# Kernel tuning notes

Measured on AMD Instinct MI355X. Metric: run time of the kernel, lower is better.

## Reference

```python
import jax, jax.numpy as jnp
import numpy as np

N_NODES = 50000
N_FEAT = 128
N_EDGES = 1600000
HID = 64


def gcn_conv(x, row, col, w, W, b, n):
    """PyG GCNConv with edge weights and added self-loops (fill_value=1).
    x: [N, Fin]; row/col: [E] (src, dst); w: [E]; W: [Fin, Fout]; b: [Fout].
    """
    loop = jnp.arange(n)
    r = jnp.concatenate([row, loop])
    c = jnp.concatenate([col, loop])
    ww = jnp.concatenate([w, jnp.ones((n,), dtype=x.dtype)])
    deg = jax.ops.segment_sum(ww, c, num_segments=n)  # [N]
    dinv = jnp.where(deg > 0, jax.lax.rsqrt(deg), 0.0)
    norm = dinv[r] * ww * dinv[c]  # [E+N]
    xw = x @ W  # [N, Fout] -- linear before propagate, as in PyG
    msg = norm[:, None] * xw[r]  # gather + scale
    out = jax.ops.segment_sum(msg, c, num_segments=n)  # scatter-add
    return out + b


def setup_inputs() -> dict:
    key = jax.random.key(0)
    ks = jax.random.split(key, 12)
    features = jax.random.normal(ks[0], (N_NODES, N_FEAT), dtype=jnp.float32)
    edge_index = jax.random.randint(ks[1], (2, N_EDGES), 0, N_NODES, dtype=jnp.int64)
    edge_attr = jax.random.uniform(ks[2], (N_EDGES,), dtype=jnp.float32)
    s = 0.05
    # generator encoder: GCNConv(n_feat->64), GCNConv(64->n_feat)
    Wg1 = jax.random.normal(ks[3], (N_FEAT, HID), dtype=jnp.float32) * s
    bg1 = jnp.zeros((HID,), dtype=jnp.float32)
    Wg2 = jax.random.normal(ks[4], (HID, N_FEAT), dtype=jnp.float32) * s
    bg2 = jnp.zeros((N_FEAT,), dtype=jnp.float32)
    # discriminator: GCNConv(n_feat->64), Linear(n_nodes*64 -> 1)
    Wd1 = jax.random.normal(ks[5], (N_FEAT, HID), dtype=jnp.float32) * s
    bd1 = jnp.zeros((HID,), dtype=jnp.float32)
    wfc = jax.random.normal(ks[6], (N_NODES * HID,), dtype=jnp.float32) * 0.001
    bfc = jnp.zeros((), dtype=jnp.float32)
    return {"features": features, "edge_index": edge_index, "edge_attr": edge_attr,
            "Wg1": Wg1, "bg1": bg1, "Wg2": Wg2, "bg2": bg2,
            "Wd1": Wd1, "bd1": bd1, "wfc": wfc, "bfc": bfc}


def reference(features, edge_index, edge_attr, Wg1, bg1, Wg2, bg2, Wd1, bd1, wfc, bfc):
    n = features.shape[0]
    row, col = edge_index[0], edge_index[1]
    # --- generator encoder (eval mode: dropout is a no-op) ---
    h = gcn_conv(features, row, col, edge_attr, Wg1, bg1, n)
    h = jax.nn.relu(h)
    z = jax.nn.sigmoid(gcn_conv(h, row, col, edge_attr, Wg2, bg2, n))  # [N, n_feat]
    # --- GAE inner-product decoder over the given edge list ---
    edge_probs = jax.nn.sigmoid(jnp.sum(z[row] * z[col], axis=-1))  # [E]
    # residual connection
    enc = z + features
    edge_probs = jnp.nan_to_num(edge_probs, nan=0.0)
    # --- discriminator (eval mode: no noise, no dropout) ---
    d = gcn_conv(enc, row, col, edge_probs, Wd1, bd1, n)
    d = jax.nn.relu(d)
    logit = jnp.dot(d.reshape(-1), wfc) + bfc
    return jax.nn.sigmoid(logit)
```

## Files before the change

### kernel.cpp

```cpp
#include <hip/hip_runtime.h>
#include <math.h>

static constexpr int NN = 50000;
static constexpr int NF = 128;
static constexpr int NH = 64;
static constexpr int NE = 1600000;
static constexpr int NBUSED = (NN + 255) / 256;
static constexpr int NWG = 256;
static constexpr int CHUNK = NE / NWG;

typedef unsigned long long u64;
typedef float f32x2 __attribute__((ext_vector_type(2)));


__device__ __forceinline__ float bf2f(unsigned u) { return __uint_as_float(u << 16); }
__device__ __forceinline__ unsigned short f2bf(float f) {
  unsigned b = __float_as_uint(f);
  b += 0x7fffu + ((b >> 16) & 1u);
  return (unsigned short)(b >> 16);
}
__device__ __forceinline__ float sigm(float x) { return 1.f / (1.f + __expf(-x)); }
__device__ __forceinline__ unsigned char f2fp8(float f) {
  int v = __builtin_amdgcn_cvt_pk_fp8_f32(f, f, 0, false);
  return (unsigned char)(v & 0xff);
}
__device__ __forceinline__ void fp8x16_dec(uint4 v, float* o) {
  f32x2 t;
  t = __builtin_amdgcn_cvt_pk_f32_fp8(v.x, false); o[0] = t.x;  o[1] = t.y;
  t = __builtin_amdgcn_cvt_pk_f32_fp8(v.x, true);  o[2] = t.x;  o[3] = t.y;
  t = __builtin_amdgcn_cvt_pk_f32_fp8(v.y, false); o[4] = t.x;  o[5] = t.y;
  t = __builtin_amdgcn_cvt_pk_f32_fp8(v.y, true);  o[6] = t.x;  o[7] = t.y;
  t = __builtin_amdgcn_cvt_pk_f32_fp8(v.z, false); o[8] = t.x;  o[9] = t.y;
  t = __builtin_amdgcn_cvt_pk_f32_fp8(v.z, true);  o[10] = t.x; o[11] = t.y;
  t = __builtin_amdgcn_cvt_pk_f32_fp8(v.w, false); o[12] = t.x; o[13] = t.y;
  t = __builtin_amdgcn_cvt_pk_f32_fp8(v.w, true);  o[14] = t.x; o[15] = t.y;
}
__device__ __forceinline__ uint4 fp8x16_enc(const float* o) {
  uint4 r;
  int v;
  v = __builtin_amdgcn_cvt_pk_fp8_f32(o[0], o[1], 0, false);
  v = __builtin_amdgcn_cvt_pk_fp8_f32(o[2], o[3], v, true);
  r.x = (unsigned)v;
  v = __builtin_amdgcn_cvt_pk_fp8_f32(o[4], o[5], 0, false);
  v = __builtin_amdgcn_cvt_pk_fp8_f32(o[6], o[7], v, true);
  r.y = (unsigned)v;
  v = __builtin_amdgcn_cvt_pk_fp8_f32(o[8], o[9], 0, false);
  v = __builtin_amdgcn_cvt_pk_fp8_f32(o[10], o[11], v, true);
  r.z = (unsigned)v;
  v = __builtin_amdgcn_cvt_pk_fp8_f32(o[12], o[13], 0, false);
  v = __builtin_amdgcn_cvt_pk_fp8_f32(o[14], o[15], v, true);
  r.w = (unsigned)v;
  return r;
}


__global__ __launch_bounds__(256) void bhist_k(const int* __restrict__ col,
                                               int* __restrict__ counts) {
  __shared__ int cnt[256];
  cnt[threadIdx.x] = 0;
  __syncthreads();
  int g = blockIdx.x;
  int e1 = g * CHUNK + CHUNK;
  for (int e = g * CHUNK + threadIdx.x; e < e1; e += 256)
    atomicAdd(&cnt[col[e] >> 8], 1);
  __syncthreads();
  counts[g * 256 + threadIdx.x] = cnt[threadIdx.x];
}

__global__ __launch_bounds__(256) void bscan_k(int* __restrict__ counts) {
  __shared__ int sm[256];
  int b = threadIdx.x;
  int tot = 0;
  for (int g = 0; g < NWG; g++) tot += counts[g * 256 + b];
  sm[b] = tot;
  __syncthreads();
  int v = tot;
  for (int off = 1; off < 256; off <<= 1) {
    int u = (b >= off) ? sm[b - off] : 0;
    __syncthreads();
    sm[b] += u;
    __syncthreads();
  }
  int run = sm[b] - v;
  for (int g = 0; g < NWG; g++) {
    int c = counts[g * 256 + b];
    counts[g * 256 + b] = run;
    run += c;
  }
}

__global__ __launch_bounds__(256) void bpart_k(const int* __restrict__ row,
                                               const int* __restrict__ col,
                                               const float* __restrict__ w,
                                               const int* __restrict__ counts,
                                               u64* __restrict__ ebuf) {
  __shared__ int cur[256];
  int g = blockIdx.x;
  cur[threadIdx.x] = counts[g * 256 + threadIdx.x];
  __syncthreads();
  int e1 = g * CHUNK + CHUNK;
  for (int e = g * CHUNK + threadIdx.x; e < e1; e += 256) {
    int c = col[e];
    int p = atomicAdd(&cur[c >> 8], 1);
    u64 pk = ((u64)(unsigned)__float_as_int(w[e]) << 32) |
             ((unsigned)(c & 255) << 16) | (unsigned)row[e];
    ebuf[p] = pk;
  }
}

__global__ __launch_bounds__(256) void bsortA_k(const u64* __restrict__ ebuf,
                                                const int* __restrict__ counts,
                                                int* __restrict__ rowstart,
                                                float* __restrict__ dinv) {
  __shared__ int cnt[256];
  __shared__ float deg[256];
  __shared__ int sm[256];
  int b = blockIdx.x, t = threadIdx.x;
  cnt[t] = 0;
  deg[t] = 1.0f;
  __syncthreads();
  int boff = counts[b];
  int bend = (b < NBUSED - 1) ? counts[b + 1] : NE;
  for (int e = boff + t; e < bend; e += 256) {
    u64 pk = ebuf[e];
    unsigned lo = (unsigned)pk;
    int c = (lo >> 16) & 255;
    atomicAdd(&cnt[c], 1);
    atomicAdd(&deg[c], __uint_as_float((unsigned)(pk >> 32)));
  }
  __syncthreads();
  int v = cnt[t];
  sm[t] = v;
  __syncthreads();
  for (int off = 1; off < 256; off <<= 1) {
    int u = (t >= off) ? sm[t - off] : 0;
    __syncthreads();
    sm[t] += u;
    __syncthreads();
  }
  int colg = b * 256 + t;
  if (colg < NN) {
    rowstart[colg] = boff + sm[t] - v;
    dinv[colg] = rsqrtf(deg[t]);
  }
  if (b == NBUSED - 1 && t == 0) rowstart[NN] = NE;
}

__global__ __launch_bounds__(256) void bsortB_k(const u64* __restrict__ ebuf,
                                                const int* __restrict__ counts,
                                                const int* __restrict__ rowstart,
                                                const float* __restrict__ dinv,
                                                int2* __restrict__ es) {
  __shared__ int cur[256];
  int b = blockIdx.x, t = threadIdx.x;
  int colg = b * 256 + t;
  cur[t] = (colg < NN) ? rowstart[colg] : NE;
  __syncthreads();
  int boff = counts[b];
  int bend = (b < NBUSED - 1) ? counts[b + 1] : NE;
  for (int e = boff + t; e < bend; e += 256) {
    u64 pk = ebuf[e];
    unsigned lo = (unsigned)pk;
    int r = lo & 0xffff;
    int c = (lo >> 16) & 255;
    float wv = __uint_as_float((unsigned)(pk >> 32));
    int p = atomicAdd(&cur[c], 1);
    es[p] = make_int2(r, __float_as_int(dinv[r] * wv));
  }
}

template<int K, int M, int ACT, bool OUTF, bool OUTH, bool XH, bool OUT8>
__global__ __launch_bounds__(256) void gemm_k(const float* __restrict__ X,
                                              const unsigned short* __restrict__ Xh,
                                              const float* __restrict__ Xadd,
                                              const float* __restrict__ W,
                                              const float* __restrict__ bias,
                                              float* __restrict__ Yf,
                                              unsigned short* __restrict__ Yh,
                                              unsigned char* __restrict__ Y8) {
  __shared__ float Ws[K * M];
  __shared__ float Xs[16][K];
  for (int i = threadIdx.x; i < K * M; i += 256) Ws[i] = W[i];
  int r0 = blockIdx.x * 16;
  for (int i = threadIdx.x; i < 16 * K; i += 256) {
    int r = i / K, k = i % K;
    size_t off = (size_t)(r0 + r) * K + k;
    float v = XH ? bf2f(Xh[off]) : X[off];
    if (Xadd) v += Xadd[off];
    Xs[r][k] = v;
  }
  __syncthreads();
  constexpr int RPT = 16 * M / 256;
  constexpr int RS = 256 / M;
  int colc = threadIdx.x % M;
  int rb = threadIdx.x / M;
  float acc[RPT];
#pragma unroll
  for (int i = 0; i < RPT; i++) acc[i] = 0.f;
  for (int k = 0; k < K; k++) {
    float wv = Ws[k * M + colc];
#pragma unroll
    for (int i = 0; i < RPT; i++) acc[i] += Xs[rb + i * RS][k] * wv;
  }
#pragma unroll
  for (int i = 0; i < RPT; i++) {
    int r = r0 + rb + i * RS;
    float o = acc[i];
    if (ACT > 0) o += bias[colc];
    if (ACT == 2) o = sigm(o);
    if (OUTF) Yf[(size_t)r * M + colc] = o;
    if (OUTH) Yh[(size_t)r * M + colc] = f2bf(o);
    if (OUT8) Y8[(size_t)r * M + colc] = f2fp8(o);
  }
}

template<int MODE>
__global__ __launch_bounds__(256) void agg64_k(const int* __restrict__ rowstart,
                                               const int2* __restrict__ es,
                                               const unsigned char* __restrict__ src8,
                                               const float* __restrict__ dinv,
                                               const float* __restrict__ bias,
                                               unsigned char* __restrict__ out8,
                                               float* __restrict__ outf,
                                               const float* __restrict__ wfc) {
  int wid = (blockIdx.x * 256 + threadIdx.x) >> 6;
  int lane = threadIdx.x & 63;
  int sub = lane >> 2;
  int l = lane & 3;
  int e0 = rowstart[wid], e1 = rowstart[wid + 1];
  float di = dinv[wid];
  float a[16];
#pragma unroll
  for (int c = 0; c < 16; c++) a[c] = 0.f;
  for (int eb = e0; eb < e1; eb += 16) {
    int e = eb + sub;
    bool valid = e < e1;
    int2 er = es[valid ? e : eb];
    float nm;
    if (MODE == 2) nm = valid ? dinv[er.x] * __int_as_float(er.y) : 0.f;
    else nm = valid ? __int_as_float(er.y) : 0.f;
    uint4 v = *(const uint4*)(src8 + (size_t)er.x * 64 + l * 16);
    float t[16];
    fp8x16_dec(v, t);
#pragma unroll
    for (int c = 0; c < 16; c++) a[c] = fmaf(nm, t[c], a[c]);
  }
#pragma unroll
  for (int c = 0; c < 16; c++) {
    a[c] += __shfl_xor(a[c], 4);
    a[c] += __shfl_xor(a[c], 8);
    a[c] += __shfl_xor(a[c], 16);
    a[c] += __shfl_xor(a[c], 32);
  }
  uint4 sv = *(const uint4*)(src8 + (size_t)wid * 64 + l * 16);
  float sf[16];
  fp8x16_dec(sv, sf);

  if (MODE == 0) {
    if (sub == 0) {
      float o[16];
#pragma unroll
      for (int c4 = 0; c4 < 4; c4++) {
        float4 b4 = *(const float4*)(bias + l * 16 + c4 * 4);
        o[c4 * 4 + 0] = fmaxf(di * (a[c4 * 4 + 0] + di * sf[c4 * 4 + 0]) + b4.x, 0.f);
        o[c4 * 4 + 1] = fmaxf(di * (a[c4 * 4 + 1] + di * sf[c4 * 4 + 1]) + b4.y, 0.f);
        o[c4 * 4 + 2] = fmaxf(di * (a[c4 * 4 + 2] + di * sf[c4 * 4 + 2]) + b4.z, 0.f);
        o[c4 * 4 + 3] = fmaxf(di * (a[c4 * 4 + 3] + di * sf[c4 * 4 + 3]) + b4.w, 0.f);
      }
      *(uint4*)(out8 + (size_t)wid * 64 + l * 16) = fp8x16_enc(o);
    }
  } else if (MODE == 1) {
    if (sub == 0) {
#pragma unroll
      for (int c4 = 0; c4 < 4; c4++) {
        float4 o4;
        o4.x = di * (a[c4 * 4 + 0] + di * sf[c4 * 4 + 0]);
        o4.y = di * (a[c4 * 4 + 1] + di * sf[c4 * 4 + 1]);
        o4.z = di * (a[c4 * 4 + 2] + di * sf[c4 * 4 + 2]);
        o4.w = di * (a[c4 * 4 + 3] + di * sf[c4 * 4 + 3]);
        *(float4*)(outf + (size_t)wid * 64 + l * 16 + c4 * 4) = o4;
      }
    }
  } else {
    float s = 0.f;
    if (sub == 0) {
#pragma unroll
      for (int c4 = 0; c4 < 4; c4++) {
        float4 b4 = *(const float4*)(bias + l * 16 + c4 * 4);
        float4 w4 = *(const float4*)(wfc + (size_t)wid * 64 + l * 16 + c4 * 4);
        float o0 = fmaxf(di * (a[c4 * 4 + 0] + di * sf[c4 * 4 + 0]) + b4.x, 0.f);
        float o1 = fmaxf(di * (a[c4 * 4 + 1] + di * sf[c4 * 4 + 1]) + b4.y, 0.f);
        float o2 = fmaxf(di * (a[c4 * 4 + 2] + di * sf[c4 * 4 + 2]) + b4.z, 0.f);
        float o3 = fmaxf(di * (a[c4 * 4 + 3] + di * sf[c4 * 4 + 3]) + b4.w, 0.f);
        s += o0 * w4.x + o1 * w4.y + o2 * w4.z + o3 * w4.w;
      }
    }
    s += __shfl_xor(s, 1);
    s += __shfl_xor(s, 2);
    __shared__ float bs[4];
    if (lane == 0) bs[threadIdx.x >> 6] = s;
    __syncthreads();
    if (threadIdx.x == 0) outf[blockIdx.x] = bs[0] + bs[1] + bs[2] + bs[3];
  }
}

__global__ __launch_bounds__(256) void eprob8_k(const int* __restrict__ rowstart,
                                                int2* __restrict__ es,
                                                const unsigned char* __restrict__ z8,
                                                float* __restrict__ dinv2) {
  int wid = (blockIdx.x * 256 + threadIdx.x) >> 6;
  int lane = threadIdx.x & 63;
  int sub = lane >> 3;
  int l = lane & 7;
  uint4 zv = *(const uint4*)(z8 + (size_t)wid * NF + l * 16);
  float zi[16];
  fp8x16_dec(zv, zi);
  int e0 = rowstart[wid], e1 = rowstart[wid + 1];
  float sum = 0.f;
  for (int eb = e0; eb < e1; eb += 8) {
    int e = eb + sub;
    bool valid = e < e1;
    int r = es[valid ? e : eb].x;
    uint4 v = *(const uint4*)(z8 + (size_t)r * NF + l * 16);
    float zr[16];
    fp8x16_dec(v, zr);
    float d = 0.f;
#pragma unroll
    for (int c = 0; c < 16; c++) d = fmaf(zr[c], zi[c], d);
    d += __shfl_xor(d, 1);
    d += __shfl_xor(d, 2);
    d += __shfl_xor(d, 4);
    if (valid && l == 0) {
      float p = sigm(d);
      es[e].y = __float_as_int(p);
      sum += p;
    }
  }
  sum += __shfl_xor(sum, 8);
  sum += __shfl_xor(sum, 16);
  sum += __shfl_xor(sum, 32);
  if (lane == 0) dinv2[wid] = rsqrtf(1.f + sum);
}

__global__ __launch_bounds__(256) void reduce_k(const float* __restrict__ partials, int n,
                                                const float* __restrict__ bfc,
                                                float* __restrict__ out) {
  float s = 0.f;
  for (int i = threadIdx.x; i < n; i += 256) s += partials[i];
  s += __shfl_xor(s, 1);
  s += __shfl_xor(s, 2);
  s += __shfl_xor(s, 4);
  s += __shfl_xor(s, 8);
  s += __shfl_xor(s, 16);
  s += __shfl_xor(s, 32);
  __shared__ float ws4[4];
  if ((threadIdx.x & 63) == 0) ws4[threadIdx.x >> 6] = s;
  __syncthreads();
  if (threadIdx.x == 0) out[0] = sigm(ws4[0] + ws4[1] + ws4[2] + ws4[3] + bfc[0]);
}


extern "C" void kernel_launch(void* const* d_in, const int* in_sizes, int n_in,
                              void* d_out, int out_size, void* d_ws, size_t ws_size,
                              hipStream_t stream) {
  const float* features = (const float*)d_in[0];
  const int* edge_index = (const int*)d_in[1];
  const float* edge_attr = (const float*)d_in[2];
  const float* Wg1 = (const float*)d_in[3];
  const float* bg1 = (const float*)d_in[4];
  const float* Wg2 = (const float*)d_in[5];
  const float* bg2 = (const float*)d_in[6];
  const float* Wd1 = (const float*)d_in[7];
  const float* bd1 = (const float*)d_in[8];
  const float* wfc = (const float*)d_in[9];
  const float* bfc = (const float*)d_in[10];
  float* out = (float*)d_out;

  const int* row = edge_index;
  const int* col = edge_index + NE;

  char* wsb = (char*)d_ws;
  auto carve = [&](size_t bytes) {
    void* p = wsb;
    wsb += (bytes + 255) & ~(size_t)255;
    return p;
  };
  int*   counts   = (int*)carve((size_t)NWG * 256 * 4);
  int*   rowstart = (int*)carve((NN + 1) * 4);
  float* dinv     = (float*)carve(NN * 4);
  float* dinv2    = (float*)carve(NN * 4);
  u64*   ebuf     = (u64*)carve((size_t)NE * 8);
  int2*  es       = (int2*)carve((size_t)NE * 8);
  unsigned char* xw8a = (unsigned char*)carve((size_t)NN * NH);
  unsigned char* hh8  = (unsigned char*)carve((size_t)NN * NH);
  float* ah   = (float*)carve((size_t)NN * NH * 4);
  unsigned short* zh = (unsigned short*)carve((size_t)NN * NF * 2);
  unsigned char* z8  = (unsigned char*)carve((size_t)NN * NF);
  unsigned char* xw8d = (unsigned char*)carve((size_t)NN * NH);
  float* partials = (float*)carve(12500 * 4);

  const int GG = NN / 16;
  const int GW = NN * 64 / 256;

  bhist_k<<<NWG, 256, 0, stream>>>(col, counts);
  bscan_k<<<1, 256, 0, stream>>>(counts);
  bpart_k<<<NWG, 256, 0, stream>>>(row, col, edge_attr, counts, ebuf);
  bsortA_k<<<NBUSED, 256, 0, stream>>>(ebuf, counts, rowstart, dinv);
  bsortB_k<<<NBUSED, 256, 0, stream>>>(ebuf, counts, rowstart, dinv, es);

  gemm_k<NF, NH, 0, false, false, false, true><<<GG, 256, 0, stream>>>(
      features, nullptr, nullptr, Wg1, nullptr, nullptr, nullptr, xw8a);
  agg64_k<0><<<GW, 256, 0, stream>>>(rowstart, es, xw8a, dinv, bg1, hh8, nullptr, nullptr);

  agg64_k<1><<<GW, 256, 0, stream>>>(rowstart, es, hh8, dinv, nullptr, nullptr, ah, nullptr);
  gemm_k<NH, NF, 2, false, true, false, true><<<GG, 256, 0, stream>>>(
      ah, nullptr, nullptr, Wg2, bg2, nullptr, zh, z8);

  eprob8_k<<<GW, 256, 0, stream>>>(rowstart, es, z8, dinv2);

  gemm_k<NF, NH, 0, false, false, true, true><<<GG, 256, 0, stream>>>(
      nullptr, zh, features, Wd1, nullptr, nullptr, nullptr, xw8d);
  agg64_k<2><<<GW, 256, 0, stream>>>(rowstart, es, xw8d, dinv2, bd1, nullptr, partials, wfc);

  reduce_k<<<1, 256, 0, stream>>>(partials, GW, bfc, out);
}
```

Before: 345.2 us.

## Pack edge records into 32 bits and assign six nodes per wave

Each sorted edge record now packs a 16-bit source index and a bf16 norm/probability into one 32-bit word instead of an int2, halving edge-stream traffic in the aggregation and edge-probability kernels. The aggregation and edge-probability kernels now have each wave loop over six consecutive destination nodes, reusing the row-start boundary and cutting launched waves and per-wave setup, with a launch-bounds occupancy hint. The trade-off is lost precision on edge weights and probabilities (bf16), and less parallelism plus more load imbalance per wave.

```diff
diff --git a/kernel.cpp b/kernel.cpp
--- a/kernel.cpp
+++ b/kernel.cpp
@@ -8,6 +8,9 @@
 static constexpr int NBUSED = (NN + 255) / 256;
 static constexpr int NWG = 256;
 static constexpr int CHUNK = NE / NWG;
+static constexpr int NPW = 6;
+static constexpr int NWAVES = (NN + NPW - 1) / NPW;
+static constexpr int GWC = (NWAVES * 64 + 255) / 256;
 
 typedef unsigned long long u64;
 typedef float f32x2 __attribute__((ext_vector_type(2)));
@@ -150,7 +153,7 @@
                                                 const int* __restrict__ counts,
                                                 const int* __restrict__ rowstart,
                                                 const float* __restrict__ dinv,
-                                                int2* __restrict__ es) {
+                                                unsigned* __restrict__ es4) {
   __shared__ int cur[256];
   int b = blockIdx.x, t = threadIdx.x;
   int colg = b * 256 + t;
@@ -165,7 +168,7 @@
     int c = (lo >> 16) & 255;
     float wv = __uint_as_float((unsigned)(pk >> 32));
     int p = atomicAdd(&cur[c], 1);
-    es[p] = make_int2(r, __float_as_int(dinv[r] * wv));
+    es4[p] = ((unsigned)f2bf(dinv[r] * wv) << 16) | (unsigned)r;
   }
 }
 
@@ -215,86 +218,96 @@
 }
 
 template<int MODE>
-__global__ __launch_bounds__(256) void agg64_k(const int* __restrict__ rowstart,
-                                               const int2* __restrict__ es,
-                                               const unsigned char* __restrict__ src8,
-                                               const float* __restrict__ dinv,
-                                               const float* __restrict__ bias,
-                                               unsigned char* __restrict__ out8,
-                                               float* __restrict__ outf,
-                                               const float* __restrict__ wfc) {
-  int wid = (blockIdx.x * 256 + threadIdx.x) >> 6;
+__global__ __launch_bounds__(256, 8) void agg64_k(const int* __restrict__ rowstart,
+                                                  const unsigned* __restrict__ es4,
+                                                  const unsigned char* __restrict__ src8,
+                                                  const float* __restrict__ dinv,
+                                                  const float* __restrict__ bias,
+                                                  unsigned char* __restrict__ out8,
+                                                  float* __restrict__ outf,
+                                                  const float* __restrict__ wfc) {
+  int w = (blockIdx.x * 256 + threadIdx.x) >> 6;
+  int n0 = w * NPW;
   int lane = threadIdx.x & 63;
   int sub = lane >> 2;
   int l = lane & 3;
-  int e0 = rowstart[wid], e1 = rowstart[wid + 1];
-  float di = dinv[wid];
-  float a[16];
-#pragma unroll
-  for (int c = 0; c < 16; c++) a[c] = 0.f;
-  for (int eb = e0; eb < e1; eb += 16) {
-    int e = eb + sub;
-    bool valid = e < e1;
-    int2 er = es[valid ? e : eb];
-    float nm;
-    if (MODE == 2) nm = valid ? dinv[er.x] * __int_as_float(er.y) : 0.f;
-    else nm = valid ? __int_as_float(er.y) : 0.f;
-    uint4 v = *(const uint4*)(src8 + (size_t)er.x * 64 + l * 16);
-    float t[16];
-    fp8x16_dec(v, t);
-#pragma unroll
-    for (int c = 0; c < 16; c++) a[c] = fmaf(nm, t[c], a[c]);
-  }
-#pragma unroll
-  for (int c = 0; c < 16; c++) {
-    a[c] += __shfl_xor(a[c], 4);
-    a[c] += __shfl_xor(a[c], 8);
-    a[c] += __shfl_xor(a[c], 16);
-    a[c] += __shfl_xor(a[c], 32);
-  }
-  uint4 sv = *(const uint4*)(src8 + (size_t)wid * 64 + l * 16);
-  float sf[16];
-  fp8x16_dec(sv, sf);
-
-  if (MODE == 0) {
-    if (sub == 0) {
-      float o[16];
-#pragma unroll
-      for (int c4 = 0; c4 < 4; c4++) {
-        float4 b4 = *(const float4*)(bias + l * 16 + c4 * 4);
-        o[c4 * 4 + 0] = fmaxf(di * (a[c4 * 4 + 0] + di * sf[c4 * 4 + 0]) + b4.x, 0.f);
-        o[c4 * 4 + 1] = fmaxf(di * (a[c4 * 4 + 1] + di * sf[c4 * 4 + 1]) + b4.y, 0.f);
-        o[c4 * 4 + 2] = fmaxf(di * (a[c4 * 4 + 2] + di * sf[c4 * 4 + 2]) + b4.z, 0.f);
-        o[c4 * 4 + 3] = fmaxf(di * (a[c4 * 4 + 3] + di * sf[c4 * 4 + 3]) + b4.w, 0.f);
+  float s = 0.f;
+  if (n0 < NN) {
+    int n1 = min(n0 + NPW, NN);
+    int e0 = rowstart[n0];
+    for (int wid = n0; wid < n1; ++wid) {
+      int e1 = rowstart[wid + 1];
+      float di = dinv[wid];
+      float a[16];
+#pragma unroll
+      for (int c = 0; c < 16; c++) a[c] = 0.f;
+      for (int eb = e0; eb < e1; eb += 16) {
+        int e = eb + sub;
+        bool valid = e < e1;
+        unsigned er = es4[valid ? e : eb];
+        int r = (int)(er & 0xffffu);
+        float nm;
+        if (MODE == 2) nm = valid ? dinv[r] * bf2f(er >> 16) : 0.f;
+        else nm = valid ? bf2f(er >> 16) : 0.f;
+        uint4 v = *(const uint4*)(src8 + (size_t)r * 64 + l * 16);
+        float t[16];
+        fp8x16_dec(v, t);
+#pragma unroll
+        for (int c = 0; c < 16; c++) a[c] = fmaf(nm, t[c], a[c]);
       }
-      *(uint4*)(out8 + (size_t)wid * 64 + l * 16) = fp8x16_enc(o);
+#pragma unroll
+      for (int c = 0; c < 16; c++) {
+        a[c] += __shfl_xor(a[c], 4);
+        a[c] += __shfl_xor(a[c], 8);
+        a[c] += __shfl_xor(a[c], 16);
+        a[c] += __shfl_xor(a[c], 32);
+      }
+      uint4 sv = *(const uint4*)(src8 + (size_t)wid * 64 + l * 16);
+      float sf[16];
+      fp8x16_dec(sv, sf);
+      if (MODE == 0) {
+        if (sub == 0) {
+          float o[16];
+#pragma unroll
+          for (int c4 = 0; c4 < 4; c4++) {
+            float4 b4 = *(const float4*)(bias + l * 16 + c4 * 4);
+            o[c4 * 4 + 0] = fmaxf(di * (a[c4 * 4 + 0] + di * sf[c4 * 4 + 0]) + b4.x, 0.f);
+            o[c4 * 4 + 1] = fmaxf(di * (a[c4 * 4 + 1] + di * sf[c4 * 4 + 1]) + b4.y, 0.f);
+            o[c4 * 4 + 2] = fmaxf(di * (a[c4 * 4 + 2] + di * sf[c4 * 4 + 2]) + b4.z, 0.f);
+            o[c4 * 4 + 3] = fmaxf(di * (a[c4 * 4 + 3] + di * sf[c4 * 4 + 3]) + b4.w, 0.f);
+          }
+          *(uint4*)(out8 + (size_t)wid * 64 + l * 16) = fp8x16_enc(o);
+        }
+      } else if (MODE == 1) {
+        if (sub == 0) {
+#pragma unroll
+          for (int c4 = 0; c4 < 4; c4++) {
+            float4 o4;
+            o4.x = di * (a[c4 * 4 + 0] + di * sf[c4 * 4 + 0]);
+            o4.y = di * (a[c4 * 4 + 1] + di * sf[c4 * 4 + 1]);
+            o4.z = di * (a[c4 * 4 + 2] + di * sf[c4 * 4 + 2]);
+            o4.w = di * (a[c4 * 4 + 3] + di * sf[c4 * 4 + 3]);
+            *(float4*)(outf + (size_t)wid * 64 + l * 16 + c4 * 4) = o4;
+          }
+        }
+      } else {
+        if (sub == 0) {
+#pragma unroll
+          for (int c4 = 0; c4 < 4; c4++) {
+            float4 b4 = *(const float4*)(bias + l * 16 + c4 * 4);
+            float4 w4 = *(const float4*)(wfc + (size_t)wid * 64 + l * 16 + c4 * 4);
+            float o0 = fmaxf(di * (a[c4 * 4 + 0] + di * sf[c4 * 4 + 0]) + b4.x, 0.f);
+            float o1 = fmaxf(di * (a[c4 * 4 + 1] + di * sf[c4 * 4 + 1]) + b4.y, 0.f);
+            float o2 = fmaxf(di * (a[c4 * 4 + 2] + di * sf[c4 * 4 + 2]) + b4.z, 0.f);
+            float o3 = fmaxf(di * (a[c4 * 4 + 3] + di * sf[c4 * 4 + 3]) + b4.w, 0.f);
+            s += o0 * w4.x + o1 * w4.y + o2 * w4.z + o3 * w4.w;
+          }
+        }
+      }
+      e0 = e1;
     }
-  } else if (MODE == 1) {
-    if (sub == 0) {
-#pragma unroll
-      for (int c4 = 0; c4 < 4; c4++) {
-        float4 o4;
-        o4.x = di * (a[c4 * 4 + 0] + di * sf[c4 * 4 + 0]);
-        o4.y = di * (a[c4 * 4 + 1] + di * sf[c4 * 4 + 1]);
-        o4.z = di * (a[c4 * 4 + 2] + di * sf[c4 * 4 + 2]);
-        o4.w = di * (a[c4 * 4 + 3] + di * sf[c4 * 4 + 3]);
-        *(float4*)(outf + (size_t)wid * 64 + l * 16 + c4 * 4) = o4;
-      }
-    }
-  } else {
-    float s = 0.f;
-    if (sub == 0) {
-#pragma unroll
-      for (int c4 = 0; c4 < 4; c4++) {
-        float4 b4 = *(const float4*)(bias + l * 16 + c4 * 4);
-        float4 w4 = *(const float4*)(wfc + (size_t)wid * 64 + l * 16 + c4 * 4);
-        float o0 = fmaxf(di * (a[c4 * 4 + 0] + di * sf[c4 * 4 + 0]) + b4.x, 0.f);
-        float o1 = fmaxf(di * (a[c4 * 4 + 1] + di * sf[c4 * 4 + 1]) + b4.y, 0.f);
-        float o2 = fmaxf(di * (a[c4 * 4 + 2] + di * sf[c4 * 4 + 2]) + b4.z, 0.f);
-        float o3 = fmaxf(di * (a[c4 * 4 + 3] + di * sf[c4 * 4 + 3]) + b4.w, 0.f);
-        s += o0 * w4.x + o1 * w4.y + o2 * w4.z + o3 * w4.w;
-      }
-    }
+  }
+  if (MODE == 2) {
     s += __shfl_xor(s, 1);
     s += __shfl_xor(s, 2);
     __shared__ float bs[4];
@@ -304,42 +317,50 @@
   }
 }
 
-__global__ __launch_bounds__(256) void eprob8_k(const int* __restrict__ rowstart,
-                                                int2* __restrict__ es,
-                                                const unsigned char* __restrict__ z8,
-                                                float* __restrict__ dinv2) {
-  int wid = (blockIdx.x * 256 + threadIdx.x) >> 6;
+__global__ __launch_bounds__(256, 8) void eprob8_k(const int* __restrict__ rowstart,
+                                                   unsigned* __restrict__ es4,
+                                                   const unsigned char* __restrict__ z8,
+                                                   float* __restrict__ dinv2) {
+  int w = (blockIdx.x * 256 + threadIdx.x) >> 6;
+  int n0 = w * NPW;
+  if (n0 >= NN) return;
+  int n1 = min(n0 + NPW, NN);
   int lane = threadIdx.x & 63;
   int sub = lane >> 3;
   int l = lane & 7;
-  uint4 zv = *(const uint4*)(z8 + (size_t)wid * NF + l * 16);
-  float zi[16];
-  fp8x16_dec(zv, zi);
-  int e0 = rowstart[wid], e1 = rowstart[wid + 1];
-  float sum = 0.f;
-  for (int eb = e0; eb < e1; eb += 8) {
-    int e = eb + sub;
-    bool valid = e < e1;
-    int r = es[valid ? e : eb].x;
-    uint4 v = *(const uint4*)(z8 + (size_t)r * NF + l * 16);
-    float zr[16];
-    fp8x16_dec(v, zr);
-    float d = 0.f;
-#pragma unroll
-    for (int c = 0; c < 16; c++) d = fmaf(zr[c], zi[c], d);
-    d += __shfl_xor(d, 1);
-    d += __shfl_xor(d, 2);
-    d += __shfl_xor(d, 4);
-    if (valid && l == 0) {
-      float p = sigm(d);
-      es[e].y = __float_as_int(p);
-      sum += p;
+  int e0 = rowstart[n0];
+  for (int wid = n0; wid < n1; ++wid) {
+    int e1 = rowstart[wid + 1];
+    uint4 zv = *(const uint4*)(z8 + (size_t)wid * NF + l * 16);
+    float zi[16];
+    fp8x16_dec(zv, zi);
+    float sum = 0.f;
+    for (int eb = e0; eb < e1; eb += 8) {
+      int e = eb + sub;
+      bool valid = e < e1;
+      unsigned er = es4[valid ? e : eb];
+      int r = (int)(er & 0xffffu);
+      uint4 v = *(const uint4*)(z8 + (size_t)r * NF + l * 16);
+      float zr[16];
+      fp8x16_dec(v, zr);
+      float d = 0.f;
+#pragma unroll
+      for (int c = 0; c < 16; c++) d = fmaf(zr[c], zi[c], d);
+      d += __shfl_xor(d, 1);
+      d += __shfl_xor(d, 2);
+      d += __shfl_xor(d, 4);
+      if (valid && l == 0) {
+        float p = sigm(d);
+        es4[e] = ((unsigned)f2bf(p) << 16) | (unsigned)r;
+        sum += p;
+      }
     }
-  }
-  sum += __shfl_xor(sum, 8);
-  sum += __shfl_xor(sum, 16);
-  sum += __shfl_xor(sum, 32);
-  if (lane == 0) dinv2[wid] = rsqrtf(1.f + sum);
+    sum += __shfl_xor(sum, 8);
+    sum += __shfl_xor(sum, 16);
+    sum += __shfl_xor(sum, 32);
+    if (lane == 0) dinv2[wid] = rsqrtf(1.f + sum);
+    e0 = e1;
+  }
 }
 
 __global__ __launch_bounds__(256) void reduce_k(const float* __restrict__ partials, int n,
@@ -390,37 +411,36 @@
   float* dinv     = (float*)carve(NN * 4);
   float* dinv2    = (float*)carve(NN * 4);
   u64*   ebuf     = (u64*)carve((size_t)NE * 8);
-  int2*  es       = (int2*)carve((size_t)NE * 8);
+  unsigned* es4   = (unsigned*)carve((size_t)NE * 4);
   unsigned char* xw8a = (unsigned char*)carve((size_t)NN * NH);
   unsigned char* hh8  = (unsigned char*)carve((size_t)NN * NH);
   float* ah   = (float*)carve((size_t)NN * NH * 4);
   unsigned short* zh = (unsigned short*)carve((size_t)NN * NF * 2);
   unsigned char* z8  = (unsigned char*)carve((size_t)NN * NF);
   unsigned char* xw8d = (unsigned char*)carve((size_t)NN * NH);
-  float* partials = (float*)carve(12500 * 4);
+  float* partials = (float*)carve((size_t)GWC * 4);
 
   const int GG = NN / 16;
-  const int GW = NN * 64 / 256;
 
   bhist_k<<<NWG, 256, 0, stream>>>(col, counts);
   bscan_k<<<1, 256, 0, stream>>>(counts);
   bpart_k<<<NWG, 256, 0, stream>>>(row, col, edge_attr, counts, ebuf);
   bsortA_k<<<NBUSED, 256, 0, stream>>>(ebuf, counts, rowstart, dinv);
-  bsortB_k<<<NBUSED, 256, 0, stream>>>(ebuf, counts, rowstart, dinv, es);
+  bsortB_k<<<NBUSED, 256, 0, stream>>>(ebuf, counts, rowstart, dinv, es4);
 
   gemm_k<NF, NH, 0, false, false, false, true><<<GG, 256, 0, stream>>>(
       features, nullptr, nullptr, Wg1, nullptr, nullptr, nullptr, xw8a);
-  agg64_k<0><<<GW, 256, 0, stream>>>(rowstart, es, xw8a, dinv, bg1, hh8, nullptr, nullptr);
-
-  agg64_k<1><<<GW, 256, 0, stream>>>(rowstart, es, hh8, dinv, nullptr, nullptr, ah, nullptr);
+  agg64_k<0><<<GWC, 256, 0, stream>>>(rowstart, es4, xw8a, dinv, bg1, hh8, nullptr, nullptr);
+
+  agg64_k<1><<<GWC, 256, 0, stream>>>(rowstart, es4, hh8, dinv, nullptr, nullptr, ah, nullptr);
   gemm_k<NH, NF, 2, false, true, false, true><<<GG, 256, 0, stream>>>(
       ah, nullptr, nullptr, Wg2, bg2, nullptr, zh, z8);
 
-  eprob8_k<<<GW, 256, 0, stream>>>(rowstart, es, z8, dinv2);
+  eprob8_k<<<GWC, 256, 0, stream>>>(rowstart, es4, z8, dinv2);
 
   gemm_k<NF, NH, 0, false, false, true, true><<<GG, 256, 0, stream>>>(
       nullptr, zh, features, Wd1, nullptr, nullptr, nullptr, xw8d);
-  agg64_k<2><<<GW, 256, 0, stream>>>(rowstart, es, xw8d, dinv2, bd1, nullptr, partials, wfc);
-
-  reduce_k<<<1, 256, 0, stream>>>(partials, GW, bfc, out);
-}
+  agg64_k<2><<<GWC, 256, 0, stream>>>(rowstart, es4, xw8d, dinv2, bd1, nullptr, partials, wfc);
+
+  reduce_k<<<1, 256, 0, stream>>>(partials, GWC, bfc, out);
+}
```

Measured after the change: 380.2 us. 10.1% more time.

## Pack edge records into 4 bytes, unroll edge loops by two, store bf16 intermediate

Applied to the files above, without the earlier changes.

Edge records shrink from an int2 (row index plus float weight) to a single 32-bit word: a 16-bit row index and a bf16 normalised weight. The aggregation and edge-probability kernels now process two edges per iteration so more gathers are in flight. The layer-2 aggregation output is written as bf16 instead of fp32, and the following GEMM reads it through its bf16 input path. The aim is to cut edge-list and intermediate memory traffic and raise memory-level parallelism, at the cost of bf16 rounding on edge weights and activations. The 16-bit index relies on the bucketed layout's local row encoding fitting in 16 bits.

```diff
diff --git a/kernel.cpp b/kernel.cpp
--- a/kernel.cpp
+++ b/kernel.cpp
@@ -150,7 +150,7 @@
                                                 const int* __restrict__ counts,
                                                 const int* __restrict__ rowstart,
                                                 const float* __restrict__ dinv,
-                                                int2* __restrict__ es) {
+                                                unsigned* __restrict__ es4) {
   __shared__ int cur[256];
   int b = blockIdx.x, t = threadIdx.x;
   int colg = b * 256 + t;
@@ -165,7 +165,7 @@
     int c = (lo >> 16) & 255;
     float wv = __uint_as_float((unsigned)(pk >> 32));
     int p = atomicAdd(&cur[c], 1);
-    es[p] = make_int2(r, __float_as_int(dinv[r] * wv));
+    es4[p] = ((unsigned)f2bf(dinv[r] * wv) << 16) | (unsigned)r;
   }
 }
 
@@ -216,11 +216,12 @@
 
 template<int MODE>
 __global__ __launch_bounds__(256) void agg64_k(const int* __restrict__ rowstart,
-                                               const int2* __restrict__ es,
+                                               const unsigned* __restrict__ es4,
                                                const unsigned char* __restrict__ src8,
                                                const float* __restrict__ dinv,
                                                const float* __restrict__ bias,
                                                unsigned char* __restrict__ out8,
+                                               unsigned short* __restrict__ outh,
                                                float* __restrict__ outf,
                                                const float* __restrict__ wfc) {
   int wid = (blockIdx.x * 256 + threadIdx.x) >> 6;
@@ -232,18 +233,31 @@
   float a[16];
 #pragma unroll
   for (int c = 0; c < 16; c++) a[c] = 0.f;
-  for (int eb = e0; eb < e1; eb += 16) {
-    int e = eb + sub;
-    bool valid = e < e1;
-    int2 er = es[valid ? e : eb];
-    float nm;
-    if (MODE == 2) nm = valid ? dinv[er.x] * __int_as_float(er.y) : 0.f;
-    else nm = valid ? __int_as_float(er.y) : 0.f;
-    uint4 v = *(const uint4*)(src8 + (size_t)er.x * 64 + l * 16);
-    float t[16];
-    fp8x16_dec(v, t);
-#pragma unroll
-    for (int c = 0; c < 16; c++) a[c] = fmaf(nm, t[c], a[c]);
+  for (int eb = e0; eb < e1; eb += 32) {
+    int eA = eb + sub;
+    int eB = eb + 16 + sub;
+    bool vA = eA < e1, vB = eB < e1;
+    unsigned erA = es4[vA ? eA : e0];
+    unsigned erB = es4[vB ? eB : e0];
+    int rA = (int)(erA & 0xffffu);
+    int rB = (int)(erB & 0xffffu);
+    float nmA, nmB;
+    if (MODE == 2) {
+      nmA = vA ? dinv[rA] * bf2f(erA >> 16) : 0.f;
+      nmB = vB ? dinv[rB] * bf2f(erB >> 16) : 0.f;
+    } else {
+      nmA = vA ? bf2f(erA >> 16) : 0.f;
+      nmB = vB ? bf2f(erB >> 16) : 0.f;
+    }
+    uint4 gA = *(const uint4*)(src8 + (size_t)rA * 64 + l * 16);
+    uint4 gB = *(const uint4*)(src8 + (size_t)rB * 64 + l * 16);
+    float tA[16], tB[16];
+    fp8x16_dec(gA, tA);
+    fp8x16_dec(gB, tB);
+#pragma unroll
+    for (int c = 0; c < 16; c++) a[c] = fmaf(nmA, tA[c], a[c]);
+#pragma unroll
+    for (int c = 0; c < 16; c++) a[c] = fmaf(nmB, tB[c], a[c]);
   }
 #pragma unroll
   for (int c = 0; c < 16; c++) {
@@ -271,15 +285,20 @@
     }
   } else if (MODE == 1) {
     if (sub == 0) {
-#pragma unroll
-      for (int c4 = 0; c4 < 4; c4++) {
-        float4 o4;
-        o4.x = di * (a[c4 * 4 + 0] + di * sf[c4 * 4 + 0]);
-        o4.y = di * (a[c4 * 4 + 1] + di * sf[c4 * 4 + 1]);
-        o4.z = di * (a[c4 * 4 + 2] + di * sf[c4 * 4 + 2]);
-        o4.w = di * (a[c4 * 4 + 3] + di * sf[c4 * 4 + 3]);
-        *(float4*)(outf + (size_t)wid * 64 + l * 16 + c4 * 4) = o4;
-      }
+      float o[16];
+#pragma unroll
+      for (int c = 0; c < 16; c++) o[c] = di * (a[c] + di * sf[c]);
+      uint4 p0, p1;
+      p0.x = (unsigned)f2bf(o[0]) | ((unsigned)f2bf(o[1]) << 16);
+      p0.y = (unsigned)f2bf(o[2]) | ((unsigned)f2bf(o[3]) << 16);
+      p0.z = (unsigned)f2bf(o[4]) | ((unsigned)f2bf(o[5]) << 16);
+      p0.w = (unsigned)f2bf(o[6]) | ((unsigned)f2bf(o[7]) << 16);
+      p1.x = (unsigned)f2bf(o[8]) | ((unsigned)f2bf(o[9]) << 16);
+      p1.y = (unsigned)f2bf(o[10]) | ((unsigned)f2bf(o[11]) << 16);
+      p1.z = (unsigned)f2bf(o[12]) | ((unsigned)f2bf(o[13]) << 16);
+      p1.w = (unsigned)f2bf(o[14]) | ((unsigned)f2bf(o[15]) << 16);
+      *(uint4*)(outh + (size_t)wid * 64 + l * 16) = p0;
+      *(uint4*)(outh + (size_t)wid * 64 + l * 16 + 8) = p1;
     }
   } else {
     float s = 0.f;
@@ -304,10 +323,10 @@
   }
 }
 
-__global__ __launch_bounds__(256) void eprob8_k(const int* __restrict__ rowstart,
-                                                int2* __restrict__ es,
-                                                const unsigned char* __restrict__ z8,
-                                                float* __restrict__ dinv2) {
+__global__ __launch_bounds__(256) void eprob16_k(const int* __restrict__ rowstart,
+                                                 unsigned* __restrict__ es4,
+                                                 const unsigned char* __restrict__ z8,
+                                                 float* __restrict__ dinv2) {
   int wid = (blockIdx.x * 256 + threadIdx.x) >> 6;
   int lane = threadIdx.x & 63;
   int sub = lane >> 3;
@@ -317,22 +336,39 @@
   fp8x16_dec(zv, zi);
   int e0 = rowstart[wid], e1 = rowstart[wid + 1];
   float sum = 0.f;
-  for (int eb = e0; eb < e1; eb += 8) {
-    int e = eb + sub;
-    bool valid = e < e1;
-    int r = es[valid ? e : eb].x;
-    uint4 v = *(const uint4*)(z8 + (size_t)r * NF + l * 16);
+  for (int eb = e0; eb < e1; eb += 16) {
+    int eA = eb + sub;
+    int eB = eb + 8 + sub;
+    bool vA = eA < e1, vB = eB < e1;
+    unsigned erA = es4[vA ? eA : e0];
+    unsigned erB = es4[vB ? eB : e0];
+    int rA = (int)(erA & 0xffffu);
+    int rB = (int)(erB & 0xffffu);
+    uint4 a4 = *(const uint4*)(z8 + (size_t)rA * NF + l * 16);
+    uint4 b4 = *(const uint4*)(z8 + (size_t)rB * NF + l * 16);
     float zr[16];
-    fp8x16_dec(v, zr);
-    float d = 0.f;
-#pragma unroll
-    for (int c = 0; c < 16; c++) d = fmaf(zr[c], zi[c], d);
-    d += __shfl_xor(d, 1);
-    d += __shfl_xor(d, 2);
-    d += __shfl_xor(d, 4);
-    if (valid && l == 0) {
-      float p = sigm(d);
-      es[e].y = __float_as_int(p);
+    fp8x16_dec(a4, zr);
+    float dA = 0.f;
+#pragma unroll
+    for (int c = 0; c < 16; c++) dA = fmaf(zr[c], zi[c], dA);
+    fp8x16_dec(b4, zr);
+    float dB = 0.f;
+#pragma unroll
+    for (int c = 0; c < 16; c++) dB = fmaf(zr[c], zi[c], dB);
+    dA += __shfl_xor(dA, 1);
+    dA += __shfl_xor(dA, 2);
+    dA += __shfl_xor(dA, 4);
+    dB += __shfl_xor(dB, 1);
+    dB += __shfl_xor(dB, 2);
+    dB += __shfl_xor(dB, 4);
+    if (vA && l == 0) {
+      float p = sigm(dA);
+      es4[eA] = ((unsigned)f2bf(p) << 16) | (unsigned)rA;
+      sum += p;
+    }
+    if (vB && l == 0) {
+      float p = sigm(dB);
+      es4[eB] = ((unsigned)f2bf(p) << 16) | (unsigned)rB;
       sum += p;
     }
   }
@@ -390,10 +426,10 @@
   float* dinv     = (float*)carve(NN * 4);
   float* dinv2    = (float*)carve(NN * 4);
   u64*   ebuf     = (u64*)carve((size_t)NE * 8);
-  int2*  es       = (int2*)carve((size_t)NE * 8);
+  unsigned* es4   = (unsigned*)carve((size_t)NE * 4);
   unsigned char* xw8a = (unsigned char*)carve((size_t)NN * NH);
   unsigned char* hh8  = (unsigned char*)carve((size_t)NN * NH);
-  float* ah   = (float*)carve((size_t)NN * NH * 4);
+  unsigned short* ahh = (unsigned short*)carve((size_t)NN * NH * 2);
   unsigned short* zh = (unsigned short*)carve((size_t)NN * NF * 2);
   unsigned char* z8  = (unsigned char*)carve((size_t)NN * NF);
   unsigned char* xw8d = (unsigned char*)carve((size_t)NN * NH);
@@ -406,21 +442,24 @@
   bscan_k<<<1, 256, 0, stream>>>(counts);
   bpart_k<<<NWG, 256, 0, stream>>>(row, col, edge_attr, counts, ebuf);
   bsortA_k<<<NBUSED, 256, 0, stream>>>(ebuf, counts, rowstart, dinv);
-  bsortB_k<<<NBUSED, 256, 0, stream>>>(ebuf, counts, rowstart, dinv, es);
+  bsortB_k<<<NBUSED, 256, 0, stream>>>(ebuf, counts, rowstart, dinv, es4);
 
   gemm_k<NF, NH, 0, false, false, false, true><<<GG, 256, 0, stream>>>(
       features, nullptr, nullptr, Wg1, nullptr, nullptr, nullptr, xw8a);
-  agg64_k<0><<<GW, 256, 0, stream>>>(rowstart, es, xw8a, dinv, bg1, hh8, nullptr, nullptr);
-
-  agg64_k<1><<<GW, 256, 0, stream>>>(rowstart, es, hh8, dinv, nullptr, nullptr, ah, nullptr);
-  gemm_k<NH, NF, 2, false, true, false, true><<<GG, 256, 0, stream>>>(
-      ah, nullptr, nullptr, Wg2, bg2, nullptr, zh, z8);
-
-  eprob8_k<<<GW, 256, 0, stream>>>(rowstart, es, z8, dinv2);
+  agg64_k<0><<<GW, 256, 0, stream>>>(rowstart, es4, xw8a, dinv, bg1, hh8, nullptr, nullptr,
+                                     nullptr);
+
+  agg64_k<1><<<GW, 256, 0, stream>>>(rowstart, es4, hh8, dinv, nullptr, nullptr, ahh, nullptr,
+                                     nullptr);
+  gemm_k<NH, NF, 2, false, true, true, true><<<GG, 256, 0, stream>>>(
+      nullptr, ahh, nullptr, Wg2, bg2, nullptr, zh, z8);
+
+  eprob16_k<<<GW, 256, 0, stream>>>(rowstart, es4, z8, dinv2);
 
   gemm_k<NF, NH, 0, false, false, true, true><<<GG, 256, 0, stream>>>(
       nullptr, zh, features, Wd1, nullptr, nullptr, nullptr, xw8d);
-  agg64_k<2><<<GW, 256, 0, stream>>>(rowstart, es, xw8d, dinv2, bd1, nullptr, partials, wfc);
+  agg64_k<2><<<GW, 256, 0, stream>>>(rowstart, es4, xw8d, dinv2, bd1, nullptr, nullptr,
+                                     partials, wfc);
 
   reduce_k<<<1, 256, 0, stream>>>(partials, GW, bfc, out);
 }
```

Result: faster. 336.7 us, median of 2 (-2.5%).
